# Optimization experiments

Measured on AMD Instinct MI355X. Metric: run time of the kernel, lower is better.

## Reference

```python
import jax, jax.numpy as jnp
import numpy as np

N = 100000   # nodes
E = 1600000  # edges
D = 128      # in_dim
H = 128      # hidden_dim
C = 40       # num_classes
EPS = 1e-5   # LayerNorm eps (torch default)


def setup_inputs() -> dict:
    key = jax.random.key(0)
    ks = jax.random.split(key, 16)
    x = jax.random.normal(ks[0], (N, D), dtype=jnp.float32)
    edge_index = jax.random.randint(ks[1], (2, E), 0, N, dtype=jnp.int64)
    s = 1.0 / np.sqrt(D)
    inp = {"x": x, "edge_index": edge_index}
    # 3 GCN layers: weight [in, H], bias [H]; LayerNorm gamma/beta [H]
    for i in range(3):
        inp[f"W{i}"] = jax.random.normal(ks[2 + i], (D if i == 0 else H, H), dtype=jnp.float32) * s
        inp[f"b{i}"] = jnp.zeros((H,), jnp.float32)
        inp[f"g{i}"] = jnp.ones((H,), jnp.float32)
        inp[f"be{i}"] = jnp.zeros((H,), jnp.float32)
    inp["Wc"] = jax.random.normal(ks[10], (H, C), dtype=jnp.float32) * (1.0 / np.sqrt(H))
    inp["bc"] = jnp.zeros((C,), jnp.float32)
    return inp


def _layer_norm(h, g, b):
    mu = jnp.mean(h, axis=-1, keepdims=True)
    var = jnp.var(h, axis=-1, keepdims=True)  # biased, matches torch
    return (h - mu) * jax.lax.rsqrt(var + EPS) * g + b


def _gcn_conv(x, W, b, src, dst, enorm, dinv2):
    # GCNConv: D^{-1/2}(A+I)D^{-1/2} X W + b (self-loops handled analytically)
    h = x @ W                                   # [N, H]
    agg = jax.ops.segment_sum(h[src] * enorm[:, None], dst, num_segments=N)
    return agg + h * dinv2[:, None] + b


def reference(x, edge_index, W0, b0, g0, be0, W1, b1, g1, be1, W2, b2, g2, be2, Wc, bc):
    src, dst = edge_index[0], edge_index[1]
    # degree with self-loops (GCNConv adds self-loops by default)
    deg = jnp.zeros((N,), x.dtype).at[dst].add(1.0) + 1.0
    dinv = jax.lax.rsqrt(deg)
    enorm = dinv[src] * dinv[dst]               # per-edge normalization
    dinv2 = dinv * dinv                         # self-loop normalization

    Ws, bs, gs, bes = (W0, W1, W2), (b0, b1, b2), (g0, g1, g2), (be0, be1, be2)
    for i in range(3):
        x_in = x
        x = _gcn_conv(x, Ws[i], bs[i], src, dst, enorm, dinv2)
        x = _layer_norm(x, gs[i], bes[i])
        x = jax.nn.elu(x)
        if i > 0:
            x = x + x_in
        # dropout: eval mode / p=0 -> identity
    return x @ Wc + bc
```

## Files before the change

### kernel.cpp

```cpp
#include <hip/hip_runtime.h>
#include <math.h>

#define N_NODES 100000
#define N_EDGES 1600000
#define DIM     128
#define NCLS    40
#define NBUCK   196
#define P1_CH   4096
#define P1_GRID 391

typedef _Float16 f16x8 __attribute__((ext_vector_type(8)));
typedef _Float16 f16x2 __attribute__((ext_vector_type(2)));
typedef float    f32x4 __attribute__((ext_vector_type(4)));

__device__ inline unsigned short f16bits(float f) {
    union { _Float16 h; unsigned short u; } cv;
    cv.h = (_Float16)f;
    return cv.u;
}
__device__ inline f16x2 as_h2(unsigned u) {
    union { unsigned u; f16x2 h; } cv;
    cv.u = u;
    return cv.h;
}
__device__ inline unsigned as_u(f16x2 h) {
    union { f16x2 h; unsigned u; } cv;
    cv.h = h;
    return cv.u;
}
__device__ inline unsigned pack_h2(float lo, float hi) {
    f16x2 h;
    h.x = (_Float16)lo;
    h.y = (_Float16)hi;
    return as_u(h);
}
__device__ inline int wave_incl_scan(int v, int lane) {
#pragma unroll
    for (int off = 1; off < 64; off <<= 1) {
        int x = __shfl_up(v, off, 64);
        if (lane >= off) v += x;
    }
    return v;
}

__global__ __launch_bounds__(256) void setup_misc(const float* __restrict__ W0,
                                                  const float* __restrict__ W1,
                                                  const float* __restrict__ W2,
                                                  const float* __restrict__ Wc,
                                                  const int* __restrict__ ei,
                                                  unsigned short* __restrict__ Wsw0,
                                                  unsigned short* __restrict__ Wsw1,
                                                  unsigned short* __restrict__ Wsw2,
                                                  unsigned short* __restrict__ Wcsw,
                                                  int* __restrict__ bcnt) {
    int blk = blockIdx.x;
    if (blk < 192) {
        const float* W = (blk < 64) ? W0 : (blk < 128) ? W1 : W2;
        unsigned short* Wsw = (blk < 64) ? Wsw0 : (blk < 128) ? Wsw1 : Wsw2;
        int o = (blk & 63) * 256 + threadIdx.x;
        int f = o >> 9;
        int l = (o >> 3) & 63;
        int j = o & 7;
        int n = f >> 2;
        int s = f & 3;
        int k = s * 32 + (l >> 4) * 8 + j;
        int c = (l & 15) * 8 + n;
        Wsw[o] = f16bits(W[k * DIM + c]);
    } else if (blk < 216) {
        int o = (blk - 192) * 256 + threadIdx.x;
        int f = o >> 9;
        int l = (o >> 3) & 63;
        int j = o & 7;
        int n = f >> 2;
        int s = f & 3;
        int k = s * 32 + (l >> 4) * 8 + j;
        int c = (l & 15) * 3 + n;
        Wcsw[o] = (c < NCLS) ? f16bits(Wc[k * NCLS + c]) : (unsigned short)0;
    } else {
        __shared__ int h[256];
        const int t  = threadIdx.x;
        const int e0 = (blk - 216) * P1_CH;
        const int cnt = min(P1_CH, N_EDGES - e0);
        h[t] = 0;
        __syncthreads();
        for (int i = t; i < cnt; i += 256)
            atomicAdd(&h[ei[N_EDGES + e0 + i] >> 9], 1);
        __syncthreads();
        if (h[t]) atomicAdd(&bcnt[t], h[t]);
    }
}

__global__ __launch_bounds__(256) void bscan(const int* __restrict__ bcnt,
                                             int* __restrict__ bbase,
                                             int* __restrict__ bcur) {
    __shared__ int wtot[4];
    int t = threadIdx.x;
    int lane = t & 63, wv = t >> 6;
    int v = (t < NBUCK) ? bcnt[t] : 0;
    int incl = wave_incl_scan(v, lane);
    if (lane == 63) wtot[wv] = incl;
    __syncthreads();
    int prefix = 0;
    for (int i = 0; i < wv; ++i) prefix += wtot[i];
    incl += prefix;
    int excl = incl - v;
    if (t < NBUCK) {
        bbase[t] = excl;
        bcur[t]  = excl;
    }
    if (t == 0) bbase[NBUCK] = N_EDGES;
}

__global__ __launch_bounds__(256) void bucket_p1(const int* __restrict__ ei,
                                                 int* __restrict__ bcur,
                                                 unsigned* __restrict__ tmp) {
    __shared__ int  hist[256];
    __shared__ int  lscan[256];
    __shared__ int  rank[256];
    __shared__ int  gbase[256];
    __shared__ int  wtot[4];
    __shared__ int2 stage[P1_CH];
    const int t  = threadIdx.x;
    const int lane = t & 63, wv = t >> 6;
    const int e0 = blockIdx.x * P1_CH;
    const int cnt = min(P1_CH, N_EDGES - e0);

    hist[t] = 0;
    __syncthreads();

    int2 ed[16];
#pragma unroll
    for (int i = 0; i < 16; ++i) {
        int idx = t + i * 256;
        if (idx < cnt) {
            int s = ei[e0 + idx];
            int d = ei[N_EDGES + e0 + idx];
            ed[i] = make_int2(s, d);
            atomicAdd(&hist[d >> 9], 1);
        }
    }
    __syncthreads();

    int hv = hist[t];
    int incl = wave_incl_scan(hv, lane);
    if (lane == 63) wtot[wv] = incl;
    __syncthreads();
    int prefix = 0;
    for (int i = 0; i < wv; ++i) prefix += wtot[i];
    incl += prefix;
    int excl = incl - hv;
    lscan[t] = excl;
    rank[t]  = excl;
    if (hv > 0) gbase[t] = atomicAdd(&bcur[t], hv);
    __syncthreads();

#pragma unroll
    for (int i = 0; i < 16; ++i) {
        int idx = t + i * 256;
        if (idx < cnt) {
            int b = ed[i].y >> 9;
            int p = atomicAdd(&rank[b], 1);
            stage[p] = ed[i];
        }
    }
    __syncthreads();

    for (int p = t; p < cnt; p += 256) {
        int2 v = stage[p];
        int b = v.y >> 9;
        tmp[gbase[b] + (p - lscan[b])] = ((unsigned)v.x << 9) | ((unsigned)v.y & 511u);
    }
}

__global__ __launch_bounds__(256) void bucket_p2a(const unsigned* __restrict__ tmp,
                                                  const int* __restrict__ bbase,
                                                  int* __restrict__ rowptr,
                                                  float* __restrict__ dinv) {
    __shared__ int cnt[512];
    __shared__ int wtot[4];
    const int t  = threadIdx.x;
    const int lane = t & 63, wv = t >> 6;
    const int b  = blockIdx.x;
    const int d0 = b << 9;
    const int dend = min(d0 + 512, N_NODES);
    const int nn = dend - d0;

    cnt[t] = 0;
    cnt[t + 256] = 0;
    __syncthreads();

    const int beg = bbase[b];
    const int end = bbase[b + 1];
    for (int idx = beg + t; idx < end; idx += 256)
        atomicAdd(&cnt[tmp[idx] & 511u], 1);
    __syncthreads();

    int c0 = cnt[2 * t];
    int c1 = cnt[2 * t + 1];
    int pv = c0 + c1;
    int incl = wave_incl_scan(pv, lane);
    if (lane == 63) wtot[wv] = incl;
    __syncthreads();
    int prefix = 0;
    for (int i = 0; i < wv; ++i) prefix += wtot[i];
    incl += prefix;
    int excl = incl - pv;
    if (2 * t < nn) {
        rowptr[d0 + 2 * t] = beg + excl;
        dinv[d0 + 2 * t]   = rsqrtf((float)c0 + 1.0f);
    }
    if (2 * t + 1 < nn) {
        rowptr[d0 + 2 * t + 1] = beg + excl + c0;
        dinv[d0 + 2 * t + 1]   = rsqrtf((float)c1 + 1.0f);
    }
    if (b == NBUCK - 1 && t == 0) rowptr[N_NODES] = N_EDGES;
}

__global__ __launch_bounds__(256) void bucket_p2b(const unsigned* __restrict__ tmp,
                                                  const int* __restrict__ rowptr,
                                                  const float* __restrict__ dinv,
                                                  int2* __restrict__ rec) {
    __shared__ int   cur[512];
    __shared__ float dinvL[512];
    const int t  = threadIdx.x;
    const int b  = blockIdx.x;
    const int d0 = b << 9;
    const int dend = min(d0 + 512, N_NODES);
    const int nn = dend - d0;

    for (int i = t; i < nn; i += 256) {
        cur[i]   = rowptr[d0 + i];
        dinvL[i] = dinv[d0 + i];
    }
    __syncthreads();

    const int beg = rowptr[d0];
    const int end = rowptr[dend];
    for (int idx = beg + t; idx < end; idx += 256) {
        unsigned u = tmp[idx];
        int s  = (int)(u >> 9);
        int dl = (int)(u & 511u);
        int pos = atomicAdd(&cur[dl], 1);
        unsigned short wb = f16bits(dinv[s] * dinvL[dl]);
        rec[pos] = make_int2(s << 8, (int)((unsigned)wb | ((unsigned)wb << 16)));
    }
}

__global__ __launch_bounds__(256) void gemm_mfma_f(const float* __restrict__ X,
                                                   const unsigned short* __restrict__ Wsw,
                                                   unsigned short* __restrict__ H) {
    __shared__ unsigned short wlds[32 * 512];
    const int tid   = threadIdx.x;
    const int lane  = tid & 63;
    const int wave  = tid >> 6;
    const int row0w = blockIdx.x * 64 + wave * 16;
    const int m = lane & 15;
    const int q = lane >> 4;

    {
        const uint4* srcp = (const uint4*)Wsw;
        uint4*       dstp = (uint4*)wlds;
#pragma unroll
        for (int i = 0; i < 8; ++i) dstp[tid + i * 256] = srcp[tid + i * 256];
    }
    __syncthreads();

    int r = row0w + m;
    if (r >= N_NODES) r = N_NODES - 1;
    const float* xp = X + (size_t)r * DIM + q * 8;
    f16x8 af[4];
#pragma unroll
    for (int s = 0; s < 4; ++s) {
        float4 x0 = *(const float4*)(xp + s * 32);
        float4 x1 = *(const float4*)(xp + s * 32 + 4);
        f16x8 v;
        v[0] = (_Float16)x0.x; v[1] = (_Float16)x0.y;
        v[2] = (_Float16)x0.z; v[3] = (_Float16)x0.w;
        v[4] = (_Float16)x1.x; v[5] = (_Float16)x1.y;
        v[6] = (_Float16)x1.z; v[7] = (_Float16)x1.w;
        af[s] = v;
    }

    f32x4 acc[8];
    f32x4 z = {0.f, 0.f, 0.f, 0.f};
#pragma unroll
    for (int n = 0; n < 8; ++n) acc[n] = z;

    const unsigned short* wl = wlds + lane * 8;
#pragma unroll
    for (int s = 0; s < 4; ++s)
#pragma unroll
        for (int n = 0; n < 8; ++n) {
            f16x8 wf = *(const f16x8*)(wl + ((n * 4 + s) << 9));
            acc[n] = __builtin_amdgcn_mfma_f32_16x16x32_f16(af[s], wf, acc[n], 0, 0, 0);
        }

#pragma unroll
    for (int j = 0; j < 4; ++j) {
        int row = row0w + q * 4 + j;
        if (row < N_NODES) {
            uint4 o;
            o.x = pack_h2(acc[0][j], acc[1][j]);
            o.y = pack_h2(acc[2][j], acc[3][j]);
            o.z = pack_h2(acc[4][j], acc[5][j]);
            o.w = pack_h2(acc[6][j], acc[7][j]);
            *(uint4*)(H + (size_t)row * DIM + m * 8) = o;
        }
    }
}

__global__ __launch_bounds__(256) void gemm_mfma_h(const unsigned short* __restrict__ Xh,
                                                   const unsigned short* __restrict__ Wsw,
                                                   unsigned short* __restrict__ H) {
    __shared__ unsigned short wlds[32 * 512];
    const int tid   = threadIdx.x;
    const int lane  = tid & 63;
    const int wave  = tid >> 6;
    const int row0w = blockIdx.x * 64 + wave * 16;
    const int m = lane & 15;
    const int q = lane >> 4;

    {
        const uint4* srcp = (const uint4*)Wsw;
        uint4*       dstp = (uint4*)wlds;
#pragma unroll
        for (int i = 0; i < 8; ++i) dstp[tid + i * 256] = srcp[tid + i * 256];
    }
    __syncthreads();

    int r = row0w + m;
    if (r >= N_NODES) r = N_NODES - 1;
    const unsigned short* xp = Xh + (size_t)r * DIM + q * 8;
    f16x8 af[4];
#pragma unroll
    for (int s = 0; s < 4; ++s) af[s] = *(const f16x8*)(xp + s * 32);

    f32x4 acc[8];
    f32x4 z = {0.f, 0.f, 0.f, 0.f};
#pragma unroll
    for (int n = 0; n < 8; ++n) acc[n] = z;

    const unsigned short* wl = wlds + lane * 8;
#pragma unroll
    for (int s = 0; s < 4; ++s)
#pragma unroll
        for (int n = 0; n < 8; ++n) {
            f16x8 wf = *(const f16x8*)(wl + ((n * 4 + s) << 9));
            acc[n] = __builtin_amdgcn_mfma_f32_16x16x32_f16(af[s], wf, acc[n], 0, 0, 0);
        }

#pragma unroll
    for (int j = 0; j < 4; ++j) {
        int row = row0w + q * 4 + j;
        if (row < N_NODES) {
            uint4 o;
            o.x = pack_h2(acc[0][j], acc[1][j]);
            o.y = pack_h2(acc[2][j], acc[3][j]);
            o.z = pack_h2(acc[4][j], acc[5][j]);
            o.w = pack_h2(acc[6][j], acc[7][j]);
            *(uint4*)(H + (size_t)row * DIM + m * 8) = o;
        }
    }
}

__global__ __launch_bounds__(256) void agg_ln(const unsigned short* __restrict__ Hh,
                                              const unsigned short* __restrict__ xin,
                                              const float* __restrict__ dinv,
                                              const float* __restrict__ bias,
                                              const float* __restrict__ g,
                                              const float* __restrict__ be,
                                              const int* __restrict__ rowptr,
                                              const int2* __restrict__ rec,
                                              unsigned short* __restrict__ outb) {
    int node = blockIdx.x * 4 + (threadIdx.x >> 6);
    int lane = threadIdx.x & 63;
    int sub  = lane & 15;
    int qtr  = lane >> 4;
    int beg = rowptr[node];
    int end = rowptr[node + 1];
    const char* Hb8 = (const char*)Hh;
    const unsigned laneoff = (unsigned)sub * 16;

    f16x2 acc[4];
    f16x2 hz = {(_Float16)0.f, (_Float16)0.f};
#pragma unroll
    for (int k = 0; k < 4; ++k) acc[k] = hz;

    for (int e0 = beg; e0 < end; e0 += 64) {
        int cnt = min(end - e0, 64);
        int2 rc = (lane < cnt) ? rec[e0 + lane] : make_int2(0, 0);
        int sv = rc.x;
        int wv = rc.y;
        int cntR = (cnt + 15) & ~15;
        for (int j = 0; j < cntR; j += 16) {
            int i0 = j + qtr, i1 = j + 4 + qtr, i2 = j + 8 + qtr, i3 = j + 12 + qtr;
            unsigned o0 = (unsigned)__shfl(sv, i0, 64) + laneoff;
            int      w0 = __shfl(wv, i0, 64);
            unsigned o1 = (unsigned)__shfl(sv, i1, 64) + laneoff;
            int      w1 = __shfl(wv, i1, 64);
            unsigned o2 = (unsigned)__shfl(sv, i2, 64) + laneoff;
            int      w2 = __shfl(wv, i2, 64);
            unsigned o3 = (unsigned)__shfl(sv, i3, 64) + laneoff;
            int      w3 = __shfl(wv, i3, 64);
            uint4 u0 = *(const uint4*)(Hb8 + o0);
            uint4 u1 = *(const uint4*)(Hb8 + o1);
            uint4 u2 = *(const uint4*)(Hb8 + o2);
            uint4 u3 = *(const uint4*)(Hb8 + o3);
            f16x2 hw0 = as_h2(w0), hw1 = as_h2(w1), hw2 = as_h2(w2), hw3 = as_h2(w3);
            acc[0] += as_h2(u0.x) * hw0;
            acc[1] += as_h2(u0.y) * hw0;
            acc[2] += as_h2(u0.z) * hw0;
            acc[3] += as_h2(u0.w) * hw0;
            acc[0] += as_h2(u1.x) * hw1;
            acc[1] += as_h2(u1.y) * hw1;
            acc[2] += as_h2(u1.z) * hw1;
            acc[3] += as_h2(u1.w) * hw1;
            acc[0] += as_h2(u2.x) * hw2;
            acc[1] += as_h2(u2.y) * hw2;
            acc[2] += as_h2(u2.z) * hw2;
            acc[3] += as_h2(u2.w) * hw2;
            acc[0] += as_h2(u3.x) * hw3;
            acc[1] += as_h2(u3.y) * hw3;
            acc[2] += as_h2(u3.z) * hw3;
            acc[3] += as_h2(u3.w) * hw3;
        }
    }

#pragma unroll
    for (int k = 0; k < 4; ++k) {
        acc[k] += as_h2(__shfl_xor(as_u(acc[k]), 16, 64));
        acc[k] += as_h2(__shfl_xor(as_u(acc[k]), 32, 64));
    }

    unsigned mu = as_u(acc[0]);
    mu = (qtr == 1) ? as_u(acc[1]) : mu;
    mu = (qtr == 2) ? as_u(acc[2]) : mu;
    mu = (qtr == 3) ? as_u(acc[3]) : mu;
    f16x2 mine = as_h2(mu);
    const int c0 = sub * 8 + qtr * 2;
    const unsigned nodeoff = ((unsigned)node << 8) + (unsigned)c0 * 2;

    float dv = dinv[node];
    float d2 = dv * dv;
    f16x2 hh = as_h2(*(const unsigned*)(Hb8 + nodeoff));
    float2 bb = *(const float2*)(bias + c0);
    float a0 = (float)mine.x + (float)hh.x * d2 + bb.x;
    float a1 = (float)mine.y + (float)hh.y * d2 + bb.y;

    float s1 = a0 + a1;
    float s2 = a0 * a0 + a1 * a1;
#pragma unroll
    for (int mk = 1; mk <= 32; mk <<= 1) {
        s1 += __shfl_xor(s1, mk, 64);
        s2 += __shfl_xor(s2, mk, 64);
    }
    float mean = s1 * (1.0f / 128.0f);
    float var  = s2 * (1.0f / 128.0f) - mean * mean;
    float rr   = rsqrtf(var + 1e-5f);
    float2 gg = *(const float2*)(g + c0);
    float2 ee = *(const float2*)(be + c0);
    float r0 = (a0 - mean) * rr * gg.x + ee.x;
    float r1 = (a1 - mean) * rr * gg.y + ee.y;
    r0 = r0 > 0.0f ? r0 : expm1f(r0);
    r1 = r1 > 0.0f ? r1 : expm1f(r1);
    if (xin) {
        f16x2 xi = as_h2(*(const unsigned*)((const char*)xin + nodeoff));
        r0 += (float)xi.x;
        r1 += (float)xi.y;
    }
    *(unsigned*)((char*)outb + nodeoff) = pack_h2(r0, r1);
}

__global__ __launch_bounds__(256) void classifier_mfma(const unsigned short* __restrict__ Xh,
                                                       const unsigned short* __restrict__ Wcsw,
                                                       const float* __restrict__ bc,
                                                       float* __restrict__ out) {
    __shared__ unsigned short wlds[12 * 512];
    const int tid   = threadIdx.x;
    const int lane  = tid & 63;
    const int wave  = tid >> 6;
    const int row0w = blockIdx.x * 128 + wave * 32;
    const int m = lane & 15;
    const int q = lane >> 4;

    {
        const uint4* srcp = (const uint4*)Wcsw;
        uint4*       dstp = (uint4*)wlds;
#pragma unroll
        for (int i = 0; i < 3; ++i) dstp[tid + i * 256] = srcp[tid + i * 256];
    }
    __syncthreads();

    f16x8 wf[12];
#pragma unroll
    for (int f = 0; f < 12; ++f)
        wf[f] = *(const f16x8*)(wlds + (f << 9) + lane * 8);

    f16x8 af[2][4];
#pragma unroll
    for (int ggr = 0; ggr < 2; ++ggr) {
        int r = row0w + ggr * 16 + m;
        if (r >= N_NODES) r = N_NODES - 1;
        const unsigned short* xp = Xh + (size_t)r * DIM + q * 8;
#pragma unroll
        for (int s = 0; s < 4; ++s) af[ggr][s] = *(const f16x8*)(xp + s * 32);
    }

    f32x4 acc[2][3];
    f32x4 z = {0.f, 0.f, 0.f, 0.f};
#pragma unroll
    for (int ggr = 0; ggr < 2; ++ggr)
#pragma unroll
        for (int n = 0; n < 3; ++n) acc[ggr][n] = z;

#pragma unroll
    for (int s = 0; s < 4; ++s)
#pragma unroll
        for (int n = 0; n < 3; ++n) {
            acc[0][n] = __builtin_amdgcn_mfma_f32_16x16x32_f16(af[0][s], wf[n * 4 + s], acc[0][n], 0, 0, 0);
            acc[1][n] = __builtin_amdgcn_mfma_f32_16x16x32_f16(af[1][s], wf[n * 4 + s], acc[1][n], 0, 0, 0);
        }

    float bcv[3];
#pragma unroll
    for (int n = 0; n < 3; ++n) {
        int c = 3 * m + n;
        bcv[n] = (c < NCLS) ? bc[c] : 0.f;
    }

#pragma unroll
    for (int ggr = 0; ggr < 2; ++ggr)
#pragma unroll
        for (int j = 0; j < 4; ++j) {
            int row = row0w + ggr * 16 + q * 4 + j;
            if (row < N_NODES) {
#pragma unroll
                for (int n = 0; n < 3; ++n) {
                    int c = 3 * m + n;
                    if (c < NCLS)
                        out[(size_t)row * NCLS + c] = acc[ggr][n][j] + bcv[n];
                }
            }
        }
}

extern "C" void kernel_launch(void* const* d_in, const int* in_sizes, int n_in,
                              void* d_out, int out_size, void* d_ws, size_t ws_size,
                              hipStream_t stream) {
    const float* x  = (const float*)d_in[0];
    const int*   ei = (const int*)d_in[1];
    const float* W[3]  = {(const float*)d_in[2], (const float*)d_in[6], (const float*)d_in[10]};
    const float* b[3]  = {(const float*)d_in[3], (const float*)d_in[7], (const float*)d_in[11]};
    const float* g[3]  = {(const float*)d_in[4], (const float*)d_in[8], (const float*)d_in[12]};
    const float* be[3] = {(const float*)d_in[5], (const float*)d_in[9], (const float*)d_in[13]};
    const float* Wc = (const float*)d_in[14];
    const float* bc = (const float*)d_in[15];
    float* out = (float*)d_out;

    char* ws = (char*)d_ws;
    const size_t NP = 400128;
    float* dinv   = (float*)(ws);
    int*   rowptr = (int*)  (ws + NP);
    int*   bcnt   = (int*)  (ws + 2 * NP);
    int*   bbase  = (int*)  (ws + 2 * NP + 1024);
    int*   bcur   = (int*)  (ws + 2 * NP + 2048);
    int2*  rec    = (int2*) (ws + 2 * NP + 4096);
    unsigned short* Hh = (unsigned short*)(ws + 2 * NP + 4096 + (size_t)N_EDGES * 8);
    unsigned short* Ah = Hh + (size_t)N_NODES * DIM;
    unsigned short* Ch = Ah + (size_t)N_NODES * DIM;
    unsigned short* Wsw0 = Ch + (size_t)N_NODES * DIM;
    unsigned short* Wsw1 = Wsw0 + DIM * DIM;
    unsigned short* Wsw2 = Wsw1 + DIM * DIM;
    unsigned short* Wcsw = Wsw2 + DIM * DIM;
    unsigned* tmp = (unsigned*)Ch;

    hipMemsetAsync(bcnt, 0, 1024, stream);
    setup_misc<<<216 + P1_GRID, 256, 0, stream>>>(W[0], W[1], W[2], Wc, ei,
                                                  Wsw0, Wsw1, Wsw2, Wcsw, bcnt);

    bscan<<<1, 256, 0, stream>>>(bcnt, bbase, bcur);
    bucket_p1<<<P1_GRID, 256, 0, stream>>>(ei, bcur, tmp);
    bucket_p2a<<<NBUCK, 256, 0, stream>>>(tmp, bbase, rowptr, dinv);
    bucket_p2b<<<NBUCK, 256, 0, stream>>>(tmp, rowptr, dinv, rec);

    const int gemm_grid = (N_NODES + 63) / 64;
    const int cls_grid  = (N_NODES + 127) / 128;
    const int agg_grid  = N_NODES / 4;

    gemm_mfma_f<<<gemm_grid, 256, 0, stream>>>(x, Wsw0, Hh);
    agg_ln<<<agg_grid, 256, 0, stream>>>(Hh, nullptr, dinv, b[0], g[0], be[0], rowptr, rec, Ch);

    gemm_mfma_h<<<gemm_grid, 256, 0, stream>>>(Ch, Wsw1, Hh);
    agg_ln<<<agg_grid, 256, 0, stream>>>(Hh, Ch, dinv, b[1], g[1], be[1], rowptr, rec, Ah);

    gemm_mfma_h<<<gemm_grid, 256, 0, stream>>>(Ah, Wsw2, Hh);
    agg_ln<<<agg_grid, 256, 0, stream>>>(Hh, Ah, dinv, b[2], g[2], be[2], rowptr, rec, Ch);

    classifier_mfma<<<cls_grid, 256, 0, stream>>>(Ch, Wcsw, bc, out);
}
```

Measured before the change: 423.0 us.

## Prescale GEMM output by dinv to drop per-edge weights from CSR records

Refactors the GCN normalization so each GEMM multiplies its output row by dinv[row], and the aggregation then just sums neighbor rows and scales by dinv[dst]. This removes the per-edge weight, halving edge record size (int2 to unsigned), and removes the f16 multiplies in the gather loop. The two bucket kernels are merged into one, skipping a launch and the rowptr/dinv reload. Padding lanes point at a sentinel zero row past N, for which Hh is enlarged and the GEMM writes zeros for out-of-range rows. Accumulating unweighted f16 sums could change rounding behaviour.

```diff
diff --git a/kernel.cpp b/kernel.cpp
--- a/kernel.cpp
+++ b/kernel.cpp
@@ -172,11 +172,13 @@
     }
 }
 
-__global__ __launch_bounds__(256) void bucket_p2a(const unsigned* __restrict__ tmp,
-                                                  const int* __restrict__ bbase,
-                                                  int* __restrict__ rowptr,
-                                                  float* __restrict__ dinv) {
+__global__ __launch_bounds__(256) void bucket_p2(const unsigned* __restrict__ tmp,
+                                                 const int* __restrict__ bbase,
+                                                 int* __restrict__ rowptr,
+                                                 float* __restrict__ dinv,
+                                                 unsigned* __restrict__ rec) {
     __shared__ int cnt[512];
+    __shared__ int cur[512];
     __shared__ int wtot[4];
     const int t  = threadIdx.x;
     const int lane = t & 63, wv = t >> 6;
@@ -205,49 +207,31 @@
     for (int i = 0; i < wv; ++i) prefix += wtot[i];
     incl += prefix;
     int excl = incl - pv;
+    int base0 = beg + excl;
+    int base1 = base0 + c0;
+    cur[2 * t]     = base0;
+    cur[2 * t + 1] = base1;
     if (2 * t < nn) {
-        rowptr[d0 + 2 * t] = beg + excl;
+        rowptr[d0 + 2 * t] = base0;
         dinv[d0 + 2 * t]   = rsqrtf((float)c0 + 1.0f);
     }
     if (2 * t + 1 < nn) {
-        rowptr[d0 + 2 * t + 1] = beg + excl + c0;
+        rowptr[d0 + 2 * t + 1] = base1;
         dinv[d0 + 2 * t + 1]   = rsqrtf((float)c1 + 1.0f);
     }
     if (b == NBUCK - 1 && t == 0) rowptr[N_NODES] = N_EDGES;
-}
-
-__global__ __launch_bounds__(256) void bucket_p2b(const unsigned* __restrict__ tmp,
-                                                  const int* __restrict__ rowptr,
-                                                  const float* __restrict__ dinv,
-                                                  int2* __restrict__ rec) {
-    __shared__ int   cur[512];
-    __shared__ float dinvL[512];
-    const int t  = threadIdx.x;
-    const int b  = blockIdx.x;
-    const int d0 = b << 9;
-    const int dend = min(d0 + 512, N_NODES);
-    const int nn = dend - d0;
-
-    for (int i = t; i < nn; i += 256) {
-        cur[i]   = rowptr[d0 + i];
-        dinvL[i] = dinv[d0 + i];
-    }
-    __syncthreads();
-
-    const int beg = rowptr[d0];
-    const int end = rowptr[dend];
+    __syncthreads();
+
     for (int idx = beg + t; idx < end; idx += 256) {
         unsigned u = tmp[idx];
-        int s  = (int)(u >> 9);
-        int dl = (int)(u & 511u);
-        int pos = atomicAdd(&cur[dl], 1);
-        unsigned short wb = f16bits(dinv[s] * dinvL[dl]);
-        rec[pos] = make_int2(s << 8, (int)((unsigned)wb | ((unsigned)wb << 16)));
+        int pos = atomicAdd(&cur[u & 511u], 1);
+        rec[pos] = (u >> 9) << 8;
     }
 }
 
 __global__ __launch_bounds__(256) void gemm_mfma_f(const float* __restrict__ X,
                                                    const unsigned short* __restrict__ Wsw,
+                                                   const float* __restrict__ dinv,
                                                    unsigned short* __restrict__ H) {
     __shared__ unsigned short wlds[32 * 512];
     const int tid   = threadIdx.x;
@@ -299,18 +283,23 @@
     for (int j = 0; j < 4; ++j) {
         int row = row0w + q * 4 + j;
         if (row < N_NODES) {
+            float dv = dinv[row];
             uint4 o;
-            o.x = pack_h2(acc[0][j], acc[1][j]);
-            o.y = pack_h2(acc[2][j], acc[3][j]);
-            o.z = pack_h2(acc[4][j], acc[5][j]);
-            o.w = pack_h2(acc[6][j], acc[7][j]);
+            o.x = pack_h2(acc[0][j] * dv, acc[1][j] * dv);
+            o.y = pack_h2(acc[2][j] * dv, acc[3][j] * dv);
+            o.z = pack_h2(acc[4][j] * dv, acc[5][j] * dv);
+            o.w = pack_h2(acc[6][j] * dv, acc[7][j] * dv);
             *(uint4*)(H + (size_t)row * DIM + m * 8) = o;
+        } else {
+            uint4 zz = make_uint4(0u, 0u, 0u, 0u);
+            *(uint4*)(H + (size_t)row * DIM + m * 8) = zz;
         }
     }
 }
 
 __global__ __launch_bounds__(256) void gemm_mfma_h(const unsigned short* __restrict__ Xh,
                                                    const unsigned short* __restrict__ Wsw,
+                                                   const float* __restrict__ dinv,
                                                    unsigned short* __restrict__ H) {
     __shared__ unsigned short wlds[32 * 512];
     const int tid   = threadIdx.x;
@@ -353,12 +342,16 @@
     for (int j = 0; j < 4; ++j) {
         int row = row0w + q * 4 + j;
         if (row < N_NODES) {
+            float dv = dinv[row];
             uint4 o;
-            o.x = pack_h2(acc[0][j], acc[1][j]);
-            o.y = pack_h2(acc[2][j], acc[3][j]);
-            o.z = pack_h2(acc[4][j], acc[5][j]);
-            o.w = pack_h2(acc[6][j], acc[7][j]);
+            o.x = pack_h2(acc[0][j] * dv, acc[1][j] * dv);
+            o.y = pack_h2(acc[2][j] * dv, acc[3][j] * dv);
+            o.z = pack_h2(acc[4][j] * dv, acc[5][j] * dv);
+            o.w = pack_h2(acc[6][j] * dv, acc[7][j] * dv);
             *(uint4*)(H + (size_t)row * DIM + m * 8) = o;
+        } else {
+            uint4 zz = make_uint4(0u, 0u, 0u, 0u);
+            *(uint4*)(H + (size_t)row * DIM + m * 8) = zz;
         }
     }
 }
@@ -370,7 +363,7 @@
                                               const float* __restrict__ g,
                                               const float* __restrict__ be,
                                               const int* __restrict__ rowptr,
-                                              const int2* __restrict__ rec,
+                                              const unsigned* __restrict__ rec,
                                               unsigned short* __restrict__ outb) {
     int node = blockIdx.x * 4 + (threadIdx.x >> 6);
     int lane = threadIdx.x & 63;
@@ -380,6 +373,7 @@
     int end = rowptr[node + 1];
     const char* Hb8 = (const char*)Hh;
     const unsigned laneoff = (unsigned)sub * 16;
+    const unsigned sentin  = (unsigned)N_NODES << 8;
 
     f16x2 acc[4];
     f16x2 hz = {(_Float16)0.f, (_Float16)0.f};
@@ -388,41 +382,33 @@
 
     for (int e0 = beg; e0 < end; e0 += 64) {
         int cnt = min(end - e0, 64);
-        int2 rc = (lane < cnt) ? rec[e0 + lane] : make_int2(0, 0);
-        int sv = rc.x;
-        int wv = rc.y;
+        unsigned sv = (lane < cnt) ? rec[e0 + lane] : sentin;
         int cntR = (cnt + 15) & ~15;
         for (int j = 0; j < cntR; j += 16) {
-            int i0 = j + qtr, i1 = j + 4 + qtr, i2 = j + 8 + qtr, i3 = j + 12 + qtr;
-            unsigned o0 = (unsigned)__shfl(sv, i0, 64) + laneoff;
-            int      w0 = __shfl(wv, i0, 64);
-            unsigned o1 = (unsigned)__shfl(sv, i1, 64) + laneoff;
-            int      w1 = __shfl(wv, i1, 64);
-            unsigned o2 = (unsigned)__shfl(sv, i2, 64) + laneoff;
-            int      w2 = __shfl(wv, i2, 64);
-            unsigned o3 = (unsigned)__shfl(sv, i3, 64) + laneoff;
-            int      w3 = __shfl(wv, i3, 64);
+            unsigned o0 = (unsigned)__shfl((int)sv, j + qtr, 64) + laneoff;
+            unsigned o1 = (unsigned)__shfl((int)sv, j + 4 + qtr, 64) + laneoff;
+            unsigned o2 = (unsigned)__shfl((int)sv, j + 8 + qtr, 64) + laneoff;
+            unsigned o3 = (unsigned)__shfl((int)sv, j + 12 + qtr, 64) + laneoff;
             uint4 u0 = *(const uint4*)(Hb8 + o0);
             uint4 u1 = *(const uint4*)(Hb8 + o1);
             uint4 u2 = *(const uint4*)(Hb8 + o2);
             uint4 u3 = *(const uint4*)(Hb8 + o3);
-            f16x2 hw0 = as_h2(w0), hw1 = as_h2(w1), hw2 = as_h2(w2), hw3 = as_h2(w3);
-            acc[0] += as_h2(u0.x) * hw0;
-            acc[1] += as_h2(u0.y) * hw0;
-            acc[2] += as_h2(u0.z) * hw0;
-            acc[3] += as_h2(u0.w) * hw0;
-            acc[0] += as_h2(u1.x) * hw1;
-            acc[1] += as_h2(u1.y) * hw1;
-            acc[2] += as_h2(u1.z) * hw1;
-            acc[3] += as_h2(u1.w) * hw1;
-            acc[0] += as_h2(u2.x) * hw2;
-            acc[1] += as_h2(u2.y) * hw2;
-            acc[2] += as_h2(u2.z) * hw2;
-            acc[3] += as_h2(u2.w) * hw2;
-            acc[0] += as_h2(u3.x) * hw3;
-            acc[1] += as_h2(u3.y) * hw3;
-            acc[2] += as_h2(u3.z) * hw3;
-            acc[3] += as_h2(u3.w) * hw3;
+            acc[0] += as_h2(u0.x);
+            acc[1] += as_h2(u0.y);
+            acc[2] += as_h2(u0.z);
+            acc[3] += as_h2(u0.w);
+            acc[0] += as_h2(u1.x);
+            acc[1] += as_h2(u1.y);
+            acc[2] += as_h2(u1.z);
+            acc[3] += as_h2(u1.w);
+            acc[0] += as_h2(u2.x);
+            acc[1] += as_h2(u2.y);
+            acc[2] += as_h2(u2.z);
+            acc[3] += as_h2(u2.w);
+            acc[0] += as_h2(u3.x);
+            acc[1] += as_h2(u3.y);
+            acc[2] += as_h2(u3.z);
+            acc[3] += as_h2(u3.w);
         }
     }
 
@@ -441,11 +427,10 @@
     const unsigned nodeoff = ((unsigned)node << 8) + (unsigned)c0 * 2;
 
     float dv = dinv[node];
-    float d2 = dv * dv;
     f16x2 hh = as_h2(*(const unsigned*)(Hb8 + nodeoff));
     float2 bb = *(const float2*)(bias + c0);
-    float a0 = (float)mine.x + (float)hh.x * d2 + bb.x;
-    float a1 = (float)mine.y + (float)hh.y * d2 + bb.y;
+    float a0 = ((float)mine.x + (float)hh.x) * dv + bb.x;
+    float a1 = ((float)mine.y + (float)hh.y) * dv + bb.y;
 
     float s1 = a0 + a1;
     float s2 = a0 * a0 + a1 * a1;
@@ -564,9 +549,9 @@
     int*   bcnt   = (int*)  (ws + 2 * NP);
     int*   bbase  = (int*)  (ws + 2 * NP + 1024);
     int*   bcur   = (int*)  (ws + 2 * NP + 2048);
-    int2*  rec    = (int2*) (ws + 2 * NP + 4096);
+    unsigned* rec = (unsigned*)(ws + 2 * NP + 4096);
     unsigned short* Hh = (unsigned short*)(ws + 2 * NP + 4096 + (size_t)N_EDGES * 8);
-    unsigned short* Ah = Hh + (size_t)N_NODES * DIM;
+    unsigned short* Ah = Hh + (size_t)(N_NODES + 64) * DIM;
     unsigned short* Ch = Ah + (size_t)N_NODES * DIM;
     unsigned short* Wsw0 = Ch + (size_t)N_NODES * DIM;
     unsigned short* Wsw1 = Wsw0 + DIM * DIM;
@@ -580,20 +565,19 @@
 
     bscan<<<1, 256, 0, stream>>>(bcnt, bbase, bcur);
     bucket_p1<<<P1_GRID, 256, 0, stream>>>(ei, bcur, tmp);
-    bucket_p2a<<<NBUCK, 256, 0, stream>>>(tmp, bbase, rowptr, dinv);
-    bucket_p2b<<<NBUCK, 256, 0, stream>>>(tmp, rowptr, dinv, rec);
+    bucket_p2<<<NBUCK, 256, 0, stream>>>(tmp, bbase, rowptr, dinv, rec);
 
     const int gemm_grid = (N_NODES + 63) / 64;
     const int cls_grid  = (N_NODES + 127) / 128;
     const int agg_grid  = N_NODES / 4;
 
-    gemm_mfma_f<<<gemm_grid, 256, 0, stream>>>(x, Wsw0, Hh);
+    gemm_mfma_f<<<gemm_grid, 256, 0, stream>>>(x, Wsw0, dinv, Hh);
     agg_ln<<<agg_grid, 256, 0, stream>>>(Hh, nullptr, dinv, b[0], g[0], be[0], rowptr, rec, Ch);
 
-    gemm_mfma_h<<<gemm_grid, 256, 0, stream>>>(Ch, Wsw1, Hh);
+    gemm_mfma_h<<<gemm_grid, 256, 0, stream>>>(Ch, Wsw1, dinv, Hh);
     agg_ln<<<agg_grid, 256, 0, stream>>>(Hh, Ch, dinv, b[1], g[1], be[1], rowptr, rec, Ah);
 
-    gemm_mfma_h<<<gemm_grid, 256, 0, stream>>>(Ah, Wsw2, Hh);
+    gemm_mfma_h<<<gemm_grid, 256, 0, stream>>>(Ah, Wsw2, dinv, Hh);
     agg_ln<<<agg_grid, 256, 0, stream>>>(Hh, Ah, dinv, b[2], g[2], be[2], rowptr, rec, Ch);
 
     classifier_mfma<<<cls_grid, 256, 0, stream>>>(Ch, Wcsw, bc, out);
```

Result: faster. 411.3 us (-2.8%).
